# Optimization experiments

Measured on AMD Instinct MI355X. Metric: run time of the kernel, lower is better.

## Reference

```python
import jax, jax.numpy as jnp
import numpy as np

# 128 molecules x 512 atoms each; batch = repeat(arange(B), NPM)
B, NPM = 128, 512
N = B * NPM
CUTOFF = 10.0
K = 32          # max_num_neighbors
BIG = 1e10      # sentinel for masked squared distances


def setup_inputs() -> dict:
    key = jax.random.key(0)
    # spread atoms so not all pairs are trivially identical
    pos = jax.random.normal(key, (N, 3), dtype=jnp.float32) * 3.0
    batch = jnp.repeat(jnp.arange(B, dtype=jnp.int32), NPM)
    return {"pos": pos, "batch": batch}


def reference(pos, batch):
    # batch is uniform blocks of size NPM (see setup_inputs), so the
    # same-molecule constraint is enforced by reshaping to [B, NPM, 3].
    p = pos.reshape(B, NPM, 3)
    sq = jnp.sum(p * p, axis=-1)                                   # [B, n]
    d2 = sq[:, :, None] + sq[:, None, :] - 2.0 * jnp.einsum(
        'bnd,bmd->bnm', p, p)                                      # [B, n, n]
    d2 = jnp.maximum(d2, 0.0)
    eye = jnp.eye(NPM, dtype=bool)
    d2m = jnp.where(eye[None] | (d2 > CUTOFF * CUTOFF), BIG, d2)
    # up to K nearest neighbors within cutoff (deterministic cap)
    neg_vals, idx = jax.lax.top_k(-d2m, K)                         # [B, n, K]
    valid = neg_vals > -0.5 * BIG
    offs = (jnp.arange(B, dtype=jnp.int32) * NPM)[:, None, None]
    dst = jnp.broadcast_to(jnp.arange(NPM, dtype=jnp.int32)[None, :, None],
                           (B, NPM, K)) + offs                     # center atom
    src = jnp.where(valid, idx.astype(jnp.int32) + offs, dst)      # pad = self-edge
    edge_weight = jnp.where(
        valid, jnp.sqrt(jnp.maximum(-neg_vals, 1e-12)), 0.0)       # ||pos_i - pos_j||
    edge_index = jnp.stack([src.reshape(-1), dst.reshape(-1)])     # [2, B*n*K]
    return edge_index, edge_weight.reshape(-1)
```

## Files before the change

kernel.cpp:

```cpp
#include <hip/hip_runtime.h>


constexpr int EDGES = 128 * 512 * 32;

static __device__ __forceinline__ unsigned umin2(unsigned a, unsigned b) {
    return a < b ? a : b;
}
static __device__ __forceinline__ unsigned umax2(unsigned a, unsigned b) {
    return a > b ? a : b;
}

static __device__ __forceinline__ unsigned mbcnt64(unsigned long long m) {
    return __builtin_amdgcn_mbcnt_hi(
        (unsigned)(m >> 32),
        __builtin_amdgcn_mbcnt_lo((unsigned)m, 0u));
}

static __device__ __forceinline__ unsigned count_lt(const unsigned q[8],
                                                    unsigned C) {
    unsigned cnt = 0;
#pragma unroll
    for (int c = 0; c < 8; ++c)
        cnt += (unsigned)__popcll(__ballot(q[c] < C));
    return cnt;
}

template <int J>
static __device__ __forceinline__ unsigned xpart(unsigned v) {
    if (J == 1) {
        return (unsigned)__builtin_amdgcn_update_dpp(
            (int)v, (int)v, 0xB1, 0xF, 0xF, false);
    } else if (J == 2) {
        return (unsigned)__builtin_amdgcn_update_dpp(
            (int)v, (int)v, 0x4E, 0xF, 0xF, false);
    }
    return (unsigned)__shfl_xor((int)v, J, 64);
}

template <int K, int J>
static __device__ __forceinline__ void bstep(unsigned& v, int lane) {
    const unsigned p = xpart<J>(v);
    const bool keepmin = (((lane & J) == 0) == ((lane & K) == 0));
    const unsigned mn = umin2(v, p);
    const unsigned mx = umax2(v, p);
    v = keepmin ? mn : mx;
}

static __device__ __forceinline__ void bitonic64(unsigned& v, int lane) {
    bstep<2, 1>(v, lane);
    bstep<4, 2>(v, lane);  bstep<4, 1>(v, lane);
    bstep<8, 4>(v, lane);  bstep<8, 2>(v, lane);  bstep<8, 1>(v, lane);
    bstep<16, 8>(v, lane); bstep<16, 4>(v, lane); bstep<16, 2>(v, lane);
    bstep<16, 1>(v, lane);
    bstep<32, 16>(v, lane); bstep<32, 8>(v, lane); bstep<32, 4>(v, lane);
    bstep<32, 2>(v, lane);  bstep<32, 1>(v, lane);
    bstep<64, 32>(v, lane); bstep<64, 16>(v, lane); bstep<64, 8>(v, lane);
    bstep<64, 4>(v, lane);  bstep<64, 2>(v, lane);  bstep<64, 1>(v, lane);
}

__global__ __launch_bounds__(256)
void RadiusInteractionGraph_73246372266582_kernel(const float* __restrict__ pos,
                                                  float* __restrict__ out) {
    __shared__ float4 atoms[512];
    __shared__ unsigned wbuf[4][2][64];

    const int tid     = threadIdx.x;
    const int b       = blockIdx.x >> 5;
    const int rowbase = (blockIdx.x & 31) * 16;
    const int base    = b * 512;

    for (int a = tid; a < 512; a += 256) {
        float x = pos[(base + a) * 3 + 0];
        float y = pos[(base + a) * 3 + 1];
        float z = pos[(base + a) * 3 + 2];
        float sq = __fadd_rn(__fadd_rn(__fmul_rn(x, x), __fmul_rn(y, y)),
                             __fmul_rn(z, z));
        atoms[a] = make_float4(x, y, z, sq);
    }
    __syncthreads();

    const int wave = tid >> 6;
    const int lane = tid & 63;

    for (int rp = 0; rp < 2; ++rp) {
        const int iA = rowbase + wave * 4 + rp * 2;
        const int iB = iA + 1;
        const float4 cA = atoms[iA];
        const float4 cB = atoms[iB];

        unsigned qA[8], qB[8];
#pragma unroll
        for (int c = 0; c < 8; ++c) {
            const int j = c * 64 + lane;
            const float4 pj = atoms[j];
            float dotA = __fadd_rn(__fadd_rn(__fmul_rn(cA.x, pj.x),
                                             __fmul_rn(cA.y, pj.y)),
                                   __fmul_rn(cA.z, pj.z));
            float dotB = __fadd_rn(__fadd_rn(__fmul_rn(cB.x, pj.x),
                                             __fmul_rn(cB.y, pj.y)),
                                   __fmul_rn(cB.z, pj.z));
            float d2A = __fsub_rn(__fadd_rn(cA.w, pj.w), __fmul_rn(2.0f, dotA));
            float d2B = __fsub_rn(__fadd_rn(cB.w, pj.w), __fmul_rn(2.0f, dotB));
            d2A = fmaxf(d2A, 0.0f);
            d2B = fmaxf(d2B, 0.0f);
            qA[c] = ((j != iA) && (d2A <= 100.0f))
                        ? ((__float_as_uint(d2A) & 0xFFFFFE00u) | (unsigned)j)
                        : (0x7F800000u | (unsigned)j);
            qB[c] = ((j != iB) && (d2B <= 100.0f))
                        ? ((__float_as_uint(d2B) & 0xFFFFFE00u) | (unsigned)j)
                        : (0x7F800000u | (unsigned)j);
        }

        unsigned XA = 0u, XB = 0u;
        for (int bit = 30; bit >= 21; --bit) {
            const unsigned CA = XA | (1u << bit);
            const unsigned CB = XB | (1u << bit);
            const unsigned ca = count_lt(qA, CA);
            const unsigned cb = count_lt(qB, CB);
            if (ca < 32u) XA = CA;
            if (cb < 32u) XB = CB;
        }
        unsigned hiA = XA + (1u << 21);
        unsigned hiB = XB + (1u << 21);
        const unsigned WA = count_lt(qA, hiA);
        const unsigned WB = count_lt(qB, hiB);
        if (WA > 64u) {
            for (int bit = 20; bit >= 0; --bit) {
                const unsigned C = XA | (1u << bit);
                if (count_lt(qA, C) < 32u) XA = C;
            }
            hiA = XA + 1u;
        }
        if (WB > 64u) {
            for (int bit = 20; bit >= 0; --bit) {
                const unsigned C = XB | (1u << bit);
                if (count_lt(qB, C) < 32u) XB = C;
            }
            hiB = XB + 1u;
        }

        wbuf[wave][0][lane] = 0xFFFFFFFFu;
        wbuf[wave][1][lane] = 0xFFFFFFFFu;
        unsigned tA = 0, tB = 0;
#pragma unroll
        for (int c = 0; c < 8; ++c) {
            const bool sA = (qA[c] < hiA);
            const bool sB = (qB[c] < hiB);
            const unsigned long long mA = __ballot(sA);
            const unsigned long long mB = __ballot(sB);
            const unsigned oA = tA + mbcnt64(mA);
            const unsigned oB = tB + mbcnt64(mB);
            if (sA) wbuf[wave][0][oA] = qA[c];
            if (sB) wbuf[wave][1][oB] = qB[c];
            tA += (unsigned)__popcll(mA);
            tB += (unsigned)__popcll(mB);
        }

        unsigned vA = wbuf[wave][0][lane];
        unsigned vB = wbuf[wave][1][lane];

        bitonic64(vA, lane);
        bitonic64(vB, lane);

        if (lane < 32) {
#pragma unroll
            for (int s = 0; s < 2; ++s) {
                const unsigned v = s ? vB : vA;
                const float4 ci = s ? cB : cA;
                const int gdst = base + (s ? iB : iA);
                float w = 0.0f;
                float srcf = (float)gdst;
                if (v < 0x7F800000u) {
                    const int j = (int)(v & 511u);
                    const float4 pj = atoms[j];
                    float dot = __fadd_rn(__fadd_rn(__fmul_rn(ci.x, pj.x),
                                                    __fmul_rn(ci.y, pj.y)),
                                          __fmul_rn(ci.z, pj.z));
                    float d2 = __fsub_rn(__fadd_rn(ci.w, pj.w),
                                         __fmul_rn(2.0f, dot));
                    d2 = fmaxf(d2, 0.0f);
                    w = __fsqrt_rn(fmaxf(d2, 1e-12f));
                    srcf = (float)(base + j);
                }
                const size_t eb = (size_t)gdst * 32 + (size_t)lane;
                out[eb]                     = srcf;
                out[(size_t)EDGES + eb]     = (float)gdst;
                out[(size_t)EDGES * 2 + eb] = w;
            }
        }
    }
}

extern "C" void kernel_launch(void* const* d_in, const int* in_sizes, int n_in,
                              void* d_out, int out_size, void* d_ws, size_t ws_size,
                              hipStream_t stream) {
    (void)in_sizes; (void)n_in; (void)d_ws; (void)ws_size; (void)out_size;
    const float* pos = (const float*)d_in[0];
    float* out       = (float*)d_out;

    RadiusInteractionGraph_73246372266582_kernel<<<dim3(4096), dim3(256), 0,
                                                   stream>>>(pos, out);
}
```

Before: 101.8 us.

## Process four rows per wave at once and use all lanes for output

Each wave now handles its four query rows in one pass instead of two passes of two rows. Sharing each atom load across four rows raises instruction-level parallelism in the distance, radix-select ballot and bitonic sort steps. The output stage moves rows 2 and 3 to the upper 32 lanes with a cross-half shuffle, so all 64 lanes write results instead of half. The cost is higher register pressure from the 32 held keys per lane, which may reduce occupancy.

```diff
diff --git a/kernel.cpp b/kernel.cpp
--- a/kernel.cpp
+++ b/kernel.cpp
@@ -16,8 +16,8 @@
         __builtin_amdgcn_mbcnt_lo((unsigned)m, 0u));
 }
 
-static __device__ __forceinline__ unsigned count_lt(const unsigned q[8],
-                                                    unsigned C) {
+static __device__ __forceinline__ unsigned count_lt8(const unsigned q[8],
+                                                     unsigned C) {
     unsigned cnt = 0;
 #pragma unroll
     for (int c = 0; c < 8; ++c)
@@ -38,31 +38,36 @@
 }
 
 template <int K, int J>
-static __device__ __forceinline__ void bstep(unsigned& v, int lane) {
-    const unsigned p = xpart<J>(v);
+static __device__ __forceinline__ void bstep4(unsigned v[4], int lane) {
+    unsigned p[4];
+#pragma unroll
+    for (int r = 0; r < 4; ++r) p[r] = xpart<J>(v[r]);
     const bool keepmin = (((lane & J) == 0) == ((lane & K) == 0));
-    const unsigned mn = umin2(v, p);
-    const unsigned mx = umax2(v, p);
-    v = keepmin ? mn : mx;
-}
-
-static __device__ __forceinline__ void bitonic64(unsigned& v, int lane) {
-    bstep<2, 1>(v, lane);
-    bstep<4, 2>(v, lane);  bstep<4, 1>(v, lane);
-    bstep<8, 4>(v, lane);  bstep<8, 2>(v, lane);  bstep<8, 1>(v, lane);
-    bstep<16, 8>(v, lane); bstep<16, 4>(v, lane); bstep<16, 2>(v, lane);
-    bstep<16, 1>(v, lane);
-    bstep<32, 16>(v, lane); bstep<32, 8>(v, lane); bstep<32, 4>(v, lane);
-    bstep<32, 2>(v, lane);  bstep<32, 1>(v, lane);
-    bstep<64, 32>(v, lane); bstep<64, 16>(v, lane); bstep<64, 8>(v, lane);
-    bstep<64, 4>(v, lane);  bstep<64, 2>(v, lane);  bstep<64, 1>(v, lane);
+#pragma unroll
+    for (int r = 0; r < 4; ++r) {
+        const unsigned mn = umin2(v[r], p[r]);
+        const unsigned mx = umax2(v[r], p[r]);
+        v[r] = keepmin ? mn : mx;
+    }
+}
+
+static __device__ __forceinline__ void bitonic64_4(unsigned v[4], int lane) {
+    bstep4<2, 1>(v, lane);
+    bstep4<4, 2>(v, lane);  bstep4<4, 1>(v, lane);
+    bstep4<8, 4>(v, lane);  bstep4<8, 2>(v, lane);  bstep4<8, 1>(v, lane);
+    bstep4<16, 8>(v, lane); bstep4<16, 4>(v, lane); bstep4<16, 2>(v, lane);
+    bstep4<16, 1>(v, lane);
+    bstep4<32, 16>(v, lane); bstep4<32, 8>(v, lane); bstep4<32, 4>(v, lane);
+    bstep4<32, 2>(v, lane);  bstep4<32, 1>(v, lane);
+    bstep4<64, 32>(v, lane); bstep4<64, 16>(v, lane); bstep4<64, 8>(v, lane);
+    bstep4<64, 4>(v, lane);  bstep4<64, 2>(v, lane);  bstep4<64, 1>(v, lane);
 }
 
 __global__ __launch_bounds__(256)
 void RadiusInteractionGraph_73246372266582_kernel(const float* __restrict__ pos,
                                                   float* __restrict__ out) {
     __shared__ float4 atoms[512];
-    __shared__ unsigned wbuf[4][2][64];
+    __shared__ unsigned wbuf[4][4][64];
 
     const int tid     = threadIdx.x;
     const int b       = blockIdx.x >> 5;
@@ -81,113 +86,117 @@
 
     const int wave = tid >> 6;
     const int lane = tid & 63;
-
-    for (int rp = 0; rp < 2; ++rp) {
-        const int iA = rowbase + wave * 4 + rp * 2;
-        const int iB = iA + 1;
-        const float4 cA = atoms[iA];
-        const float4 cB = atoms[iB];
-
-        unsigned qA[8], qB[8];
+    const int i0   = rowbase + (wave << 2);
+
+    const float4 c0 = atoms[i0 + 0];
+    const float4 c1 = atoms[i0 + 1];
+    const float4 c2 = atoms[i0 + 2];
+    const float4 c3 = atoms[i0 + 3];
+
+    unsigned q[4][8];
+#pragma unroll
+    for (int c = 0; c < 8; ++c) {
+        const int j = c * 64 + lane;
+        const float4 pj = atoms[j];
+#pragma unroll
+        for (int r = 0; r < 4; ++r) {
+            const float4 ci = (r == 0) ? c0 : (r == 1) ? c1 : (r == 2) ? c2 : c3;
+            float dot = __fadd_rn(__fadd_rn(__fmul_rn(ci.x, pj.x),
+                                            __fmul_rn(ci.y, pj.y)),
+                                  __fmul_rn(ci.z, pj.z));
+            float d2 = __fsub_rn(__fadd_rn(ci.w, pj.w), __fmul_rn(2.0f, dot));
+            d2 = fmaxf(d2, 0.0f);
+            q[r][c] = ((j != i0 + r) && (d2 <= 100.0f))
+                          ? ((__float_as_uint(d2) & 0xFFFFFE00u) | (unsigned)j)
+                          : (0x7F800000u | (unsigned)j);
+        }
+    }
+
+    unsigned X[4] = {0u, 0u, 0u, 0u};
+    for (int bit = 30; bit >= 21; --bit) {
+        unsigned C[4];
+#pragma unroll
+        for (int r = 0; r < 4; ++r) C[r] = X[r] | (1u << bit);
+        unsigned n0 = 0, n1 = 0, n2 = 0, n3 = 0;
 #pragma unroll
         for (int c = 0; c < 8; ++c) {
-            const int j = c * 64 + lane;
+            n0 += (unsigned)__popcll(__ballot(q[0][c] < C[0]));
+            n1 += (unsigned)__popcll(__ballot(q[1][c] < C[1]));
+            n2 += (unsigned)__popcll(__ballot(q[2][c] < C[2]));
+            n3 += (unsigned)__popcll(__ballot(q[3][c] < C[3]));
+        }
+        if (n0 < 32u) X[0] = C[0];
+        if (n1 < 32u) X[1] = C[1];
+        if (n2 < 32u) X[2] = C[2];
+        if (n3 < 32u) X[3] = C[3];
+    }
+
+    unsigned hi[4], W[4];
+#pragma unroll
+    for (int r = 0; r < 4; ++r) {
+        hi[r] = X[r] + (1u << 21);
+        W[r]  = count_lt8(q[r], hi[r]);
+    }
+#pragma unroll
+    for (int r = 0; r < 4; ++r) {
+        if (W[r] > 64u) {
+            for (int bit = 20; bit >= 0; --bit) {
+                const unsigned C = X[r] | (1u << bit);
+                if (count_lt8(q[r], C) < 32u) X[r] = C;
+            }
+            hi[r] = X[r] + 1u;
+        }
+    }
+
+#pragma unroll
+    for (int r = 0; r < 4; ++r) wbuf[wave][r][lane] = 0xFFFFFFFFu;
+    unsigned t[4] = {0u, 0u, 0u, 0u};
+#pragma unroll
+    for (int c = 0; c < 8; ++c) {
+#pragma unroll
+        for (int r = 0; r < 4; ++r) {
+            const bool s = (q[r][c] < hi[r]);
+            const unsigned long long m = __ballot(s);
+            const unsigned o = t[r] + mbcnt64(m);
+            if (s) wbuf[wave][r][o] = q[r][c];
+            t[r] += (unsigned)__popcll(m);
+        }
+    }
+
+    unsigned v[4];
+#pragma unroll
+    for (int r = 0; r < 4; ++r) v[r] = wbuf[wave][r][lane];
+
+    bitonic64_4(v, lane);
+
+    const unsigned vu2 = (unsigned)__shfl_xor((int)v[2], 32, 64);
+    const unsigned vu3 = (unsigned)__shfl_xor((int)v[3], 32, 64);
+    const int half = lane >> 5;
+    const int l32  = lane & 31;
+#pragma unroll
+    for (int s = 0; s < 2; ++s) {
+        const unsigned vv = half ? (s ? vu3 : vu2) : (s ? v[1] : v[0]);
+        const int gi   = i0 + (half << 1) + s;
+        const int gdst = base + gi;
+        const float4 ci = atoms[gi];
+        float w = 0.0f;
+        float srcf = (float)gdst;
+        if (vv < 0x7F800000u) {
+            const int j = (int)(vv & 511u);
             const float4 pj = atoms[j];
-            float dotA = __fadd_rn(__fadd_rn(__fmul_rn(cA.x, pj.x),
-                                             __fmul_rn(cA.y, pj.y)),
-                                   __fmul_rn(cA.z, pj.z));
-            float dotB = __fadd_rn(__fadd_rn(__fmul_rn(cB.x, pj.x),
-                                             __fmul_rn(cB.y, pj.y)),
-                                   __fmul_rn(cB.z, pj.z));
-            float d2A = __fsub_rn(__fadd_rn(cA.w, pj.w), __fmul_rn(2.0f, dotA));
-            float d2B = __fsub_rn(__fadd_rn(cB.w, pj.w), __fmul_rn(2.0f, dotB));
-            d2A = fmaxf(d2A, 0.0f);
-            d2B = fmaxf(d2B, 0.0f);
-            qA[c] = ((j != iA) && (d2A <= 100.0f))
-                        ? ((__float_as_uint(d2A) & 0xFFFFFE00u) | (unsigned)j)
-                        : (0x7F800000u | (unsigned)j);
-            qB[c] = ((j != iB) && (d2B <= 100.0f))
-                        ? ((__float_as_uint(d2B) & 0xFFFFFE00u) | (unsigned)j)
-                        : (0x7F800000u | (unsigned)j);
-        }
-
-        unsigned XA = 0u, XB = 0u;
-        for (int bit = 30; bit >= 21; --bit) {
-            const unsigned CA = XA | (1u << bit);
-            const unsigned CB = XB | (1u << bit);
-            const unsigned ca = count_lt(qA, CA);
-            const unsigned cb = count_lt(qB, CB);
-            if (ca < 32u) XA = CA;
-            if (cb < 32u) XB = CB;
-        }
-        unsigned hiA = XA + (1u << 21);
-        unsigned hiB = XB + (1u << 21);
-        const unsigned WA = count_lt(qA, hiA);
-        const unsigned WB = count_lt(qB, hiB);
-        if (WA > 64u) {
-            for (int bit = 20; bit >= 0; --bit) {
-                const unsigned C = XA | (1u << bit);
-                if (count_lt(qA, C) < 32u) XA = C;
-            }
-            hiA = XA + 1u;
-        }
-        if (WB > 64u) {
-            for (int bit = 20; bit >= 0; --bit) {
-                const unsigned C = XB | (1u << bit);
-                if (count_lt(qB, C) < 32u) XB = C;
-            }
-            hiB = XB + 1u;
-        }
-
-        wbuf[wave][0][lane] = 0xFFFFFFFFu;
-        wbuf[wave][1][lane] = 0xFFFFFFFFu;
-        unsigned tA = 0, tB = 0;
-#pragma unroll
-        for (int c = 0; c < 8; ++c) {
-            const bool sA = (qA[c] < hiA);
-            const bool sB = (qB[c] < hiB);
-            const unsigned long long mA = __ballot(sA);
-            const unsigned long long mB = __ballot(sB);
-            const unsigned oA = tA + mbcnt64(mA);
-            const unsigned oB = tB + mbcnt64(mB);
-            if (sA) wbuf[wave][0][oA] = qA[c];
-            if (sB) wbuf[wave][1][oB] = qB[c];
-            tA += (unsigned)__popcll(mA);
-            tB += (unsigned)__popcll(mB);
-        }
-
-        unsigned vA = wbuf[wave][0][lane];
-        unsigned vB = wbuf[wave][1][lane];
-
-        bitonic64(vA, lane);
-        bitonic64(vB, lane);
-
-        if (lane < 32) {
-#pragma unroll
-            for (int s = 0; s < 2; ++s) {
-                const unsigned v = s ? vB : vA;
-                const float4 ci = s ? cB : cA;
-                const int gdst = base + (s ? iB : iA);
-                float w = 0.0f;
-                float srcf = (float)gdst;
-                if (v < 0x7F800000u) {
-                    const int j = (int)(v & 511u);
-                    const float4 pj = atoms[j];
-                    float dot = __fadd_rn(__fadd_rn(__fmul_rn(ci.x, pj.x),
-                                                    __fmul_rn(ci.y, pj.y)),
-                                          __fmul_rn(ci.z, pj.z));
-                    float d2 = __fsub_rn(__fadd_rn(ci.w, pj.w),
-                                         __fmul_rn(2.0f, dot));
-                    d2 = fmaxf(d2, 0.0f);
-                    w = __fsqrt_rn(fmaxf(d2, 1e-12f));
-                    srcf = (float)(base + j);
-                }
-                const size_t eb = (size_t)gdst * 32 + (size_t)lane;
-                out[eb]                     = srcf;
-                out[(size_t)EDGES + eb]     = (float)gdst;
-                out[(size_t)EDGES * 2 + eb] = w;
-            }
-        }
+            float dot = __fadd_rn(__fadd_rn(__fmul_rn(ci.x, pj.x),
+                                            __fmul_rn(ci.y, pj.y)),
+                                  __fmul_rn(ci.z, pj.z));
+            float d2 = __fsub_rn(__fadd_rn(ci.w, pj.w),
+                                 __fmul_rn(2.0f, dot));
+            d2 = fmaxf(d2, 0.0f);
+            w = __fsqrt_rn(fmaxf(d2, 1e-12f));
+            srcf = (float)(base + j);
+        }
+        const size_t eb = (size_t)gdst * 32 + (size_t)l32;
+        out[eb]                     = srcf;
+        out[(size_t)EDGES + eb]     = (float)gdst;
+        out[(size_t)EDGES * 2 + eb] = w;
     }
 }
 
```

Result: slower. 112.5 us (+10.6%).
